# Optimization experiments

Hardware: AMD Instinct MI355X
Metric: run time of the kernel (lower is better)

## Reference

```python
import jax, jax.numpy as jnp
import numpy as np

D_K = 32
TOPK_FRAC = 0.1
DROP_P = 0.1


def setup_inputs() -> dict:
    key = jax.random.key(0)
    k1, k2, k3, k4 = jax.random.split(key, 4)
    B, F, N, T = 4, 64, 4096, 12
    dim = T * F  # 768
    x = jax.random.normal(k1, (B, F, N, T), dtype=jnp.float32)
    # nn.Linear(dim, d_k, bias=False): y = x @ W.T ; store W transposed as [dim, d_k]
    W_Q = jax.random.normal(k2, (dim, D_K), dtype=jnp.float32) * (1.0 / np.sqrt(dim))
    W_K = jax.random.normal(k3, (dim, D_K), dtype=jnp.float32) * (1.0 / np.sqrt(dim))
    # uniform noise driving F.dropout (training=True) deterministically
    drop_u = jax.random.uniform(k4, (N, N), dtype=jnp.float32)
    return {"x": x, "W_Q": W_Q, "W_K": W_K, "drop_u": drop_u}


def _drop(attn, drop_u):
    # k = int(N*N*0.1); topk over flattened matrix
    N, M = attn.shape
    k = int(N * M * TOPK_FRAC)
    flat = attn.reshape(-1)
    _, idx = jax.lax.top_k(flat, k)
    topk_mask = jnp.zeros_like(flat).at[idx].set(1.0).reshape(N, M)
    kept = attn * topk_mask
    # F.dropout on the remainder: zero with prob p, scale survivors by 1/(1-p)
    keep = (drop_u >= DROP_P).astype(attn.dtype)
    remaining = attn * (1.0 - topk_mask) * keep * (1.0 / (1.0 - DROP_P))
    return kept + remaining


def reference(x, W_Q, W_K, drop_u):
    B, F, N, T = x.shape
    # [B, F, N, T] -> [B, N, T, F] -> [B, N, T*F]
    xr = jnp.transpose(x, (0, 2, 3, 1)).reshape(B, N, T * F)
    Q = xr @ W_Q  # [B, N, d_k]
    K = xr @ W_K  # [B, N, d_k]
    scores = jnp.einsum("bnd,bmd->bnm", Q, K) * (1.0 / np.sqrt(D_K))  # [B, N, N]
    attn = jax.nn.softmax(jnp.sum(scores, axis=0), axis=-1)  # [N, N]
    return _drop(attn, drop_u)
```

## Files before the change

### kernel.cpp

```cpp
#include <hip/hip_runtime.h>
#include <stdint.h>

#define NN 4096
#define KSEL_S 419430u
#define INV_SQRT_DK 0.17677669529663687f

#define OFF_QH 0u
#define OFF_KH (1u<<20)
#define OFF_STATS (2u<<20)
#define OFF_H   (3u<<20)
#define OFF_H2  (4u<<20)
#define OFF_ST  ((4u<<20) + 65536u)
#define OFF_MASK (5u<<20)
#define OFF_SB  (16u<<20)
#define WS_NEED_B16 (48u<<20)

#define LDB 104

typedef __attribute__((ext_vector_type(8))) short bf16x8;
typedef __attribute__((ext_vector_type(8))) unsigned short u16x8;
typedef __attribute__((ext_vector_type(4))) float f32x4;

static __device__ __forceinline__ short f2bf(float f) {
    unsigned u = __float_as_uint(f);
    unsigned r = (u + 0x7FFFu + ((u >> 16) & 1u)) >> 16;
    return (short)r;
}
static __device__ __forceinline__ float bf2f(short h) {
    return __uint_as_float(((unsigned)(unsigned short)h) << 16);
}

__global__ __launch_bounds__(256) void proj_kernel(
    const float* __restrict__ x, const float* __restrict__ WQ,
    const float* __restrict__ WK,
    short* __restrict__ Qh, short* __restrict__ Kh)
{
    __shared__ short Ah[2][64 * LDB];
    __shared__ short Al[2][64 * LDB];
    __shared__ short Bl[2][64 * LDB];
    const int bx  = blockIdx.x;
    const int b   = bx >> 6;
    const int n0  = (bx & 63) << 6;
    const int tid = threadIdx.x;
    const int l   = tid & 63;
    const int w   = __builtin_amdgcn_readfirstlane(tid >> 6);
    const int lr  = l & 15;
    const int kg  = (l >> 4) * 8;

    f32x4 acc[4];
#pragma unroll
    for (int j = 0; j < 4; ++j) acc[j] = (f32x4){0.f, 0.f, 0.f, 0.f};

    auto STAGE = [&](int c, int sbuf) {
#pragma unroll
        for (int j = 0; j < 6; ++j) {
            const int s   = tid + (j << 8);
            const int f_l = s / 192;
            const int rem = s - f_l * 192;
            const int r   = rem / 3;
            const int t4  = rem - r * 3;
            float4 v = *(const float4*)(x + (size_t)b * 3145728
                                          + (size_t)(c * 8 + f_l) * 49152
                                          + (size_t)(n0 + r) * 12 + t4 * 4);
            const int kl = f_l * 12 + t4 * 4;
            short4 hi, lo;
            hi.x = f2bf(v.x); lo.x = f2bf(v.x - bf2f(hi.x));
            hi.y = f2bf(v.y); lo.y = f2bf(v.y - bf2f(hi.y));
            hi.z = f2bf(v.z); lo.z = f2bf(v.z - bf2f(hi.z));
            hi.w = f2bf(v.w); lo.w = f2bf(v.w - bf2f(hi.w));
            *(short4*)&Ah[sbuf][r * LDB + kl] = hi;
            *(short4*)&Al[sbuf][r * LDB + kl] = lo;
        }
#pragma unroll
        for (int j = 0; j < 6; ++j) {
            const int s   = tid + (j << 8);
            const int qk  = (s >= 768) ? 1 : 0;
            const int rem = s - qk * 768;
            const int kr  = rem >> 3;
            const int c4  = rem & 7;
            const int t   = kr % 12;
            const int f_l = kr / 12;
            const float* __restrict__ Wp = qk ? WK : WQ;
            float4 wv = *(const float4*)(Wp + (size_t)(t * 64 + c * 8 + f_l) * 32 + (c4 << 2));
            const int kl = f_l * 12 + t;
            const int col = (qk << 5) + (c4 << 2);
            Bl[sbuf][(col + 0) * LDB + kl] = f2bf(wv.x);
            Bl[sbuf][(col + 1) * LDB + kl] = f2bf(wv.y);
            Bl[sbuf][(col + 2) * LDB + kl] = f2bf(wv.z);
            Bl[sbuf][(col + 3) * LDB + kl] = f2bf(wv.w);
        }
    };

    STAGE(0, 0);
    int buf = 0;
    for (int c = 0; c < 8; ++c) {
        __syncthreads();
        if (c < 7) STAGE(c + 1, buf ^ 1);
#pragma unroll
        for (int ks = 0; ks < 3; ++ks) {
            const int ko = ks * 32 + kg;
            bf16x8 ah = *(const bf16x8*)&Ah[buf][(w * 16 + lr) * LDB + ko];
            bf16x8 al = *(const bf16x8*)&Al[buf][(w * 16 + lr) * LDB + ko];
#pragma unroll
            for (int j = 0; j < 4; ++j) {
                bf16x8 bb = *(const bf16x8*)&Bl[buf][(j * 16 + lr) * LDB + ko];
                acc[j] = __builtin_amdgcn_mfma_f32_16x16x32_bf16(ah, bb, acc[j], 0, 0, 0);
                acc[j] = __builtin_amdgcn_mfma_f32_16x16x32_bf16(al, bb, acc[j], 0, 0, 0);
            }
        }
        buf ^= 1;
    }

#pragma unroll
    for (int j = 0; j < 4; ++j) {
        const int col = j * 16 + lr;
#pragma unroll
        for (int r = 0; r < 4; ++r) {
            const int row = n0 + w * 16 + (l >> 4) * 4 + r;
            if (col < 32)
                Qh[(size_t)row * 128 + (b << 5) + col] = f2bf(acc[j][r] * INV_SQRT_DK);
            else
                Kh[(size_t)row * 128 + (b << 5) + (col - 32)] = f2bf(acc[j][r]);
        }
    }
}

__global__ __launch_bounds__(256) void mask_kernel(
    const float4* __restrict__ u4, unsigned* __restrict__ maskw)
{
    const unsigned word = blockIdx.x * 256 + threadIdx.x;
    const float4* __restrict__ up = u4 + (size_t)word * 8;
    unsigned m = 0;
#pragma unroll
    for (int j = 0; j < 8; ++j) {
        float4 a = up[j];
        m |= (a.x >= 0.1f ? 1u : 0u) << (4 * j);
        m |= (a.y >= 0.1f ? 2u : 0u) << (4 * j);
        m |= (a.z >= 0.1f ? 4u : 0u) << (4 * j);
        m |= (a.w >= 0.1f ? 8u : 0u) << (4 * j);
    }
    maskw[word] = m;
}

template<bool B16>
__global__ __launch_bounds__(256, 3) void gemm_kernel(
    const short* __restrict__ Qh, const short* __restrict__ Kh, void* Sv)
{
    const int bi = blockIdx.x >> 5, bj = blockIdx.x & 31;
    const int tid = threadIdx.x;
    const int w = tid >> 6, l = tid & 63;
    const int m0 = bi * 128 + (w >> 1) * 64;
    const int n0 = bj * 128 + (w & 1) * 64;
    const int lr = l & 15;
    const int kg = (l >> 4) * 8;

    f32x4 acc[4][4];
#pragma unroll
    for (int i = 0; i < 4; ++i)
#pragma unroll
        for (int j = 0; j < 4; ++j) acc[i][j] = (f32x4){0.f, 0.f, 0.f, 0.f};

    bf16x8 aA[4], bA[4], aB[4], bB[4];

    auto LD = [&](bf16x8* A, bf16x8* B, int k0) {
#pragma unroll
        for (int i = 0; i < 4; ++i) {
            A[i] = *(const bf16x8*)(Qh + (size_t)(m0 + i * 16 + lr) * 128 + k0 + kg);
            B[i] = *(const bf16x8*)(Kh + (size_t)(n0 + i * 16 + lr) * 128 + k0 + kg);
        }
    };
    auto DOMFMA = [&](bf16x8* A, bf16x8* B) {
#pragma unroll
        for (int i = 0; i < 4; ++i)
#pragma unroll
            for (int j = 0; j < 4; ++j)
                acc[i][j] = __builtin_amdgcn_mfma_f32_16x16x32_bf16(A[i], B[j], acc[i][j], 0, 0, 0);
    };

    LD(aA, bA, 0);
    LD(aB, bB, 32);
    DOMFMA(aA, bA);  LD(aA, bA, 64);
    DOMFMA(aB, bB);  LD(aB, bB, 96);
    DOMFMA(aA, bA);
    DOMFMA(aB, bB);

#pragma unroll
    for (int i = 0; i < 4; ++i) {
        int rowb = m0 + i * 16 + (l >> 4) * 4;
#pragma unroll
        for (int j = 0; j < 4; ++j) {
            int col = n0 + j * 16 + (l & 15);
#pragma unroll
            for (int r = 0; r < 4; ++r) {
                if constexpr (B16)
                    ((unsigned short*)Sv)[(size_t)(rowb + r) * NN + col] =
                        (unsigned short)f2bf(acc[i][j][r]);
                else
                    ((float*)Sv)[(size_t)(rowb + r) * NN + col] = acc[i][j][r];
            }
        }
    }
}

template<bool B16>
__global__ __launch_bounds__(512) void histstat_kernel(
    const void* __restrict__ Sv, float2* __restrict__ stats,
    unsigned* __restrict__ gh)
{
    __shared__ unsigned h[1024];
    const int tid = threadIdx.x;
    const int l = tid & 63;
    const int w = tid >> 6;

    for (int i = tid; i < 1024; i += 512) h[i] = 0;
    __syncthreads();

#pragma unroll
    for (int r = 0; r < 2; ++r) {
        const int row = (blockIdx.x << 4) + (r << 3) + w;

        float v[64];
        if constexpr (B16) {
            const u16x8* rp = (const u16x8*)((const unsigned short*)Sv + (size_t)row * NN);
#pragma unroll
            for (int j = 0; j < 8; ++j) {
                u16x8 e = rp[l + (j << 6)];
#pragma unroll
                for (int i = 0; i < 8; ++i) v[j * 8 + i] = bf2f((short)e[i]);
            }
        } else {
            const float4* rp = (const float4*)((const float*)Sv + (size_t)row * NN);
#pragma unroll
            for (int j = 0; j < 16; ++j) {
                float4 t = rp[l + (j << 6)];
                v[j * 4 + 0] = t.x; v[j * 4 + 1] = t.y;
                v[j * 4 + 2] = t.z; v[j * 4 + 3] = t.w;
            }
        }

        float s = 0.f;
#pragma unroll
        for (int j = 0; j < 64; ++j) { v[j] = __expf(v[j]); s += v[j]; }
#pragma unroll
        for (int off = 32; off; off >>= 1) s += __shfl_xor(s, off);
        const float inv = 1.0f / s;
        if (l == 0) stats[row] = make_float2(0.f, inv);

        if constexpr (B16) {
#pragma unroll
            for (int jj = 0; jj < 2; ++jj) {
                const int base = jj * 32;
#pragma unroll
                for (int c = 0; c < 8; ++c) {
                    int b0 = min(max((int)(__float_as_uint(v[base + c] * inv) >> 16) - 0x3780, 0), 1023);
                    atomicAdd(&h[b0], 1u);
                }
            }
        } else {
#pragma unroll
            for (int jj = 0; jj < 4; ++jj) {
                const int base = jj * 16;
#pragma unroll
                for (int c = 0; c < 4; ++c) {
                    int b0 = min(max((int)(__float_as_uint(v[base + c] * inv) >> 16) - 0x3780, 0), 1023);
                    atomicAdd(&h[b0], 1u);
                }
            }
        }
    }

    __syncthreads();
    unsigned* dst = gh + ((unsigned)blockIdx.x << 10);
    for (int i = tid; i < 1024; i += 512) dst[i] = h[i];
}

__global__ __launch_bounds__(1024) void reduce_kernel(
    const unsigned* __restrict__ gh, unsigned* __restrict__ gh2)
{
    const int t = threadIdx.x, b = blockIdx.x;
    unsigned s = 0;
    for (int p = 0; p < 32; ++p) s += gh[((unsigned)(b * 32 + p) << 10) + t];
    gh2[((unsigned)b << 10) + t] = s;
}

__global__ __launch_bounds__(1024) void scan_kernel(
    const unsigned* __restrict__ gh2, unsigned* st)
{
    __shared__ unsigned P[1024];
    const int t = threadIdx.x;
    unsigned s = 0;
#pragma unroll
    for (int p = 0; p < 8; ++p) s += gh2[(p << 10) + t];
    P[t] = s;
    __syncthreads();
    for (int off = 1; off < 1024; off <<= 1) {
        unsigned v = P[t] + ((t + off < 1024) ? P[t + off] : 0u);
        __syncthreads();
        P[t] = v;
        __syncthreads();
    }
    if (P[t] >= KSEL_S && (t == 1023 || P[t + 1] < KSEL_S))
        st[2] = (0x3780u + (unsigned)t) << 16;
}

template<bool B16>
__global__ __launch_bounds__(256) void final_kernel(
    const void* __restrict__ Sv, float* __restrict__ out,
    const unsigned* __restrict__ maskw,
    const float2* __restrict__ stats, const unsigned* __restrict__ st)
{
    const int row = blockIdx.x;
    const int tid = threadIdx.x;
    const float thr = __uint_as_float(st[2]);
    const float2 stt = stats[row];
    float4* o4 = (float4*)(out + (size_t)row * NN);
    const unsigned* mw = maskw + (size_t)row * 128;

    float4 sv[4];
    unsigned wv[4];

    if constexpr (B16) {
        const ushort4* S4 = (const ushort4*)((const unsigned short*)Sv + (size_t)row * NN);
        ushort4 sraw[4];
#pragma unroll
        for (int j = 0; j < 4; ++j) sraw[j] = S4[tid + (j << 8)];
#pragma unroll
        for (int j = 0; j < 4; ++j) wv[j] = mw[(tid >> 3) + (j << 5)];
#pragma unroll
        for (int j = 0; j < 4; ++j) {
            sv[j].x = bf2f((short)sraw[j].x); sv[j].y = bf2f((short)sraw[j].y);
            sv[j].z = bf2f((short)sraw[j].z); sv[j].w = bf2f((short)sraw[j].w);
        }
    } else {
        const float4* S4 = (const float4*)((const float*)Sv + (size_t)row * NN);
#pragma unroll
        for (int j = 0; j < 4; ++j) sv[j] = S4[tid + (j << 8)];
#pragma unroll
        for (int j = 0; j < 4; ++j) wv[j] = mw[(tid >> 3) + (j << 5)];
    }

    const unsigned sh = (tid & 7) << 2;
#pragma unroll
    for (int j = 0; j < 4; ++j) {
        const unsigned bits = (wv[j] >> sh) & 0xFu;
        float4 o;
        float p;
        p = __expf(sv[j].x - stt.x) * stt.y;
        o.x = (p >= thr) ? p : ((bits & 1u) ? p * (1.0f / 0.9f) : 0.0f);
        p = __expf(sv[j].y - stt.x) * stt.y;
        o.y = (p >= thr) ? p : ((bits & 2u) ? p * (1.0f / 0.9f) : 0.0f);
        p = __expf(sv[j].z - stt.x) * stt.y;
        o.z = (p >= thr) ? p : ((bits & 4u) ? p * (1.0f / 0.9f) : 0.0f);
        p = __expf(sv[j].w - stt.x) * stt.y;
        o.w = (p >= thr) ? p : ((bits & 8u) ? p * (1.0f / 0.9f) : 0.0f);
        o4[tid + (j << 8)] = o;
    }
}

extern "C" void kernel_launch(void* const* d_in, const int* in_sizes, int n_in,
                              void* d_out, int out_size, void* d_ws, size_t ws_size,
                              hipStream_t stream)
{
    const float* x  = (const float*)d_in[0];
    const float* WQ = (const float*)d_in[1];
    const float* WK = (const float*)d_in[2];
    const float* du = (const float*)d_in[3];
    float* out = (float*)d_out;
    char* ws = (char*)d_ws;

    short* Qh = (short*)(ws + OFF_QH);
    short* Kh = (short*)(ws + OFF_KH);
    float2* stats = (float2*)(ws + OFF_STATS);
    unsigned* hist = (unsigned*)(ws + OFF_H);
    unsigned* gh2  = (unsigned*)(ws + OFF_H2);
    unsigned* st   = (unsigned*)(ws + OFF_ST);
    unsigned* mask = (unsigned*)(ws + OFF_MASK);

    proj_kernel<<<256, 256, 0, stream>>>(x, WQ, WK, Qh, Kh);
    mask_kernel<<<2048, 256, 0, stream>>>((const float4*)du, mask);

    const bool b16 = (ws_size >= (size_t)WS_NEED_B16);
    if (b16) {
        void* Sb = (void*)(ws + OFF_SB);
        gemm_kernel<true><<<1024, 256, 0, stream>>>(Qh, Kh, Sb);
        histstat_kernel<true><<<256, 512, 0, stream>>>(Sb, stats, hist);
        reduce_kernel<<<8, 1024, 0, stream>>>(hist, gh2);
        scan_kernel<<<1, 1024, 0, stream>>>(gh2, st);
        final_kernel<true><<<NN, 256, 0, stream>>>(Sb, out, mask, stats, st);
    } else {
        gemm_kernel<false><<<1024, 256, 0, stream>>>(Qh, Kh, (void*)out);
        histstat_kernel<false><<<256, 512, 0, stream>>>((void*)out, stats, hist);
        reduce_kernel<<<8, 1024, 0, stream>>>(hist, gh2);
        scan_kernel<<<1, 1024, 0, stream>>>(gh2, st);
        final_kernel<false><<<NN, 256, 0, stream>>>((void*)out, out, mask, stats, st);
    }
}
```

Before: 84.93 us.

## Fuse row exp-sum into GEMM epilogue and shrink histogram row reads

The GEMM epilogue now computes per-row partial sums of exp(score) for each 128-column tile and writes them to a workspace array. The histogram kernel reduces these 32 partials per row to get the softmax normaliser. It then only loads the sampled subset of each row it histograms, instead of the whole row. This removes most of the score-matrix reads and exp work from the histogram pass, in exchange for extra exp, shuffles and shared atomics in the GEMM epilogue.

```diff
diff --git a/kernel.cpp b/kernel.cpp
--- a/kernel.cpp
+++ b/kernel.cpp
@@ -12,6 +12,7 @@
 #define OFF_H2  (4u<<20)
 #define OFF_ST  ((4u<<20) + 65536u)
 #define OFF_MASK (5u<<20)
+#define OFF_PS  (6u<<20)
 #define OFF_SB  (16u<<20)
 #define WS_NEED_B16 (48u<<20)
 
@@ -144,8 +145,10 @@
 
 template<bool B16>
 __global__ __launch_bounds__(256, 3) void gemm_kernel(
-    const short* __restrict__ Qh, const short* __restrict__ Kh, void* Sv)
-{
+    const short* __restrict__ Qh, const short* __restrict__ Kh, void* Sv,
+    float* __restrict__ Psum)
+{
+    __shared__ float rsum[128];
     const int bi = blockIdx.x >> 5, bj = blockIdx.x & 31;
     const int tid = threadIdx.x;
     const int w = tid >> 6, l = tid & 63;
@@ -184,6 +187,8 @@
     DOMFMA(aA, bA);
     DOMFMA(aB, bB);
 
+    for (int t = tid; t < 128; t += 256) rsum[t] = 0.f;
+
 #pragma unroll
     for (int i = 0; i < 4; ++i) {
         int rowb = m0 + i * 16 + (l >> 4) * 4;
@@ -200,72 +205,84 @@
             }
         }
     }
+
+    __syncthreads();
+#pragma unroll
+    for (int i = 0; i < 4; ++i) {
+#pragma unroll
+        for (int r = 0; r < 4; ++r) {
+            float vs = 0.f;
+#pragma unroll
+            for (int j = 0; j < 4; ++j) {
+                float sval;
+                if constexpr (B16) sval = bf2f(f2bf(acc[i][j][r]));
+                else               sval = acc[i][j][r];
+                vs += __expf(sval);
+            }
+#pragma unroll
+            for (int off = 1; off < 16; off <<= 1) vs += __shfl_xor(vs, off);
+            if ((l & 15) == 0)
+                atomicAdd(&rsum[(w >> 1) * 64 + i * 16 + (l >> 4) * 4 + r], vs);
+        }
+    }
+    __syncthreads();
+    if (tid < 128)
+        Psum[(size_t)(bi * 128 + tid) * 32 + bj] = rsum[tid];
 }
 
 template<bool B16>
-__global__ __launch_bounds__(512) void histstat_kernel(
-    const void* __restrict__ Sv, float2* __restrict__ stats,
-    unsigned* __restrict__ gh)
+__global__ __launch_bounds__(512) void hist_kernel(
+    const void* __restrict__ Sv, const float* __restrict__ Psum,
+    float2* __restrict__ stats, unsigned* __restrict__ gh)
 {
     __shared__ unsigned h[1024];
+    __shared__ float rinv[16];
     const int tid = threadIdx.x;
     const int l = tid & 63;
     const int w = tid >> 6;
 
     for (int i = tid; i < 1024; i += 512) h[i] = 0;
+
+    {
+        const int rl = tid >> 5, p = tid & 31;
+        float v = Psum[(size_t)((blockIdx.x << 4) + rl) * 32 + p];
+#pragma unroll
+        for (int off = 1; off < 32; off <<= 1) v += __shfl_xor(v, off);
+        if (p == 0) {
+            const float inv = 1.0f / v;
+            rinv[rl] = inv;
+            stats[(blockIdx.x << 4) + rl] = make_float2(0.f, inv);
+        }
+    }
     __syncthreads();
 
 #pragma unroll
     for (int r = 0; r < 2; ++r) {
-        const int row = (blockIdx.x << 4) + (r << 3) + w;
-
-        float v[64];
+        const int rl  = (r << 3) + w;
+        const int row = (blockIdx.x << 4) + rl;
+        const float inv = rinv[rl];
+
+        float v[16];
         if constexpr (B16) {
             const u16x8* rp = (const u16x8*)((const unsigned short*)Sv + (size_t)row * NN);
-#pragma unroll
-            for (int j = 0; j < 8; ++j) {
-                u16x8 e = rp[l + (j << 6)];
-#pragma unroll
-                for (int i = 0; i < 8; ++i) v[j * 8 + i] = bf2f((short)e[i]);
-            }
+            u16x8 e0 = rp[l];
+            u16x8 e1 = rp[l + 64];
+#pragma unroll
+            for (int i = 0; i < 8; ++i) { v[i] = bf2f((short)e0[i]); v[8 + i] = bf2f((short)e1[i]); }
         } else {
             const float4* rp = (const float4*)((const float*)Sv + (size_t)row * NN);
 #pragma unroll
-            for (int j = 0; j < 16; ++j) {
-                float4 t = rp[l + (j << 6)];
-                v[j * 4 + 0] = t.x; v[j * 4 + 1] = t.y;
-                v[j * 4 + 2] = t.z; v[j * 4 + 3] = t.w;
+            for (int j = 0; j < 4; ++j) {
+                float4 t4 = rp[l + (j << 6)];
+                v[j * 4 + 0] = t4.x; v[j * 4 + 1] = t4.y;
+                v[j * 4 + 2] = t4.z; v[j * 4 + 3] = t4.w;
             }
         }
-
-        float s = 0.f;
-#pragma unroll
-        for (int j = 0; j < 64; ++j) { v[j] = __expf(v[j]); s += v[j]; }
-#pragma unroll
-        for (int off = 32; off; off >>= 1) s += __shfl_xor(s, off);
-        const float inv = 1.0f / s;
-        if (l == 0) stats[row] = make_float2(0.f, inv);
-
-        if constexpr (B16) {
-#pragma unroll
-            for (int jj = 0; jj < 2; ++jj) {
-                const int base = jj * 32;
-#pragma unroll
-                for (int c = 0; c < 8; ++c) {
-                    int b0 = min(max((int)(__float_as_uint(v[base + c] * inv) >> 16) - 0x3780, 0), 1023);
-                    atomicAdd(&h[b0], 1u);
-                }
-            }
-        } else {
-#pragma unroll
-            for (int jj = 0; jj < 4; ++jj) {
-                const int base = jj * 16;
-#pragma unroll
-                for (int c = 0; c < 4; ++c) {
-                    int b0 = min(max((int)(__float_as_uint(v[base + c] * inv) >> 16) - 0x3780, 0), 1023);
-                    atomicAdd(&h[b0], 1u);
-                }
-            }
+#pragma unroll
+        for (int i = 0; i < 16; ++i) {
+            float p = __expf(v[i]) * inv;
+            int b0 = min(max((int)(__float_as_uint(p) >> 16) - 0x3780, 0), 1023);
+            atomicAdd(&h[b0], 1u);
         }
     }
 
@@ -375,6 +392,7 @@
     unsigned* gh2  = (unsigned*)(ws + OFF_H2);
     unsigned* st   = (unsigned*)(ws + OFF_ST);
     unsigned* mask = (unsigned*)(ws + OFF_MASK);
+    float* Psum    = (float*)(ws + OFF_PS);
 
     proj_kernel<<<256, 256, 0, stream>>>(x, WQ, WK, Qh, Kh);
     mask_kernel<<<2048, 256, 0, stream>>>((const float4*)du, mask);
@@ -382,14 +400,14 @@
     const bool b16 = (ws_size >= (size_t)WS_NEED_B16);
     if (b16) {
         void* Sb = (void*)(ws + OFF_SB);
-        gemm_kernel<true><<<1024, 256, 0, stream>>>(Qh, Kh, Sb);
-        histstat_kernel<true><<<256, 512, 0, stream>>>(Sb, stats, hist);
+        gemm_kernel<true><<<1024, 256, 0, stream>>>(Qh, Kh, Sb, Psum);
+        hist_kernel<true><<<256, 512, 0, stream>>>(Sb, Psum, stats, hist);
         reduce_kernel<<<8, 1024, 0, stream>>>(hist, gh2);
         scan_kernel<<<1, 1024, 0, stream>>>(gh2, st);
         final_kernel<true><<<NN, 256, 0, stream>>>(Sb, out, mask, stats, st);
     } else {
-        gemm_kernel<false><<<1024, 256, 0, stream>>>(Qh, Kh, (void*)out);
-        histstat_kernel<false><<<256, 512, 0, stream>>>((void*)out, stats, hist);
+        gemm_kernel<false><<<1024, 256, 0, stream>>>(Qh, Kh, (void*)out, Psum);
+        hist_kernel<false><<<256, 512, 0, stream>>>((void*)out, Psum, stats, hist);
         reduce_kernel<<<8, 1024, 0, stream>>>(hist, gh2);
         scan_kernel<<<1, 1024, 0, stream>>>(gh2, st);
         final_kernel<false><<<NN, 256, 0, stream>>>((void*)out, out, mask, stats, st);
```

After: 90.59 us. 1.07x slower.
